# Kernel optimization log

Measured on AMD Instinct MI355X. Metric: run time of the kernel, lower is better.

## Reference

```python
import jax, jax.numpy as jnp
from jax import lax
import numpy as np

BN_EPS = 1e-5


def _dwconv3x3(x, w):
    # x: [B,C,H,W], w: [C,1,3,3] depthwise (groups == C)
    return lax.conv_general_dilated(
        x, w, window_strides=(1, 1), padding='SAME',
        dimension_numbers=('NCHW', 'OIHW', 'NCHW'),
        feature_group_count=x.shape[1])


def _bn_eval(x, g, b, m, v):
    s = g * lax.rsqrt(v + BN_EPS)            # [C]
    return x * s[None, :, None, None] + (b - m * s)[None, :, None, None]


def _maxpool2(x):
    return lax.reduce_window(x, -jnp.inf, lax.max,
                             (1, 1, 2, 2), (1, 1, 2, 2), 'VALID')


def setup_inputs() -> dict:
    key = jax.random.key(0)
    ks = jax.random.split(key, 8)
    B, Cin, H, W = 32, 128, 64, 64
    Hd = 256               # hidden_size
    K, Ck = 32, 8          # num categories, hidden_size // K
    sc = 0.05
    return {
        'v4_features': jax.random.normal(ks[0], (B, Cin, H, W), jnp.float32),
        'w1_dw': jax.random.normal(ks[1], (Cin, 1, 3, 3), jnp.float32) * sc,
        'w1_pw': jax.random.normal(ks[2], (Hd, Cin), jnp.float32) * sc,
        'bn1_g': jnp.ones((Hd,), jnp.float32),
        'bn1_b': jnp.zeros((Hd,), jnp.float32),
        'bn1_m': jnp.zeros((Hd,), jnp.float32),
        'bn1_v': jnp.ones((Hd,), jnp.float32),
        'w2_dw': jax.random.normal(ks[3], (Hd, 1, 3, 3), jnp.float32) * sc,
        'w2_pw': jax.random.normal(ks[4], (Hd, Hd), jnp.float32) * sc,
        'bn2_g': jnp.ones((Hd,), jnp.float32),
        'bn2_b': jnp.zeros((Hd,), jnp.float32),
        'bn2_m': jnp.zeros((Hd,), jnp.float32),
        'bn2_v': jnp.ones((Hd,), jnp.float32),
        'cat_w': jax.random.normal(ks[5], (K, Ck, Hd), jnp.float32) * sc,
        'emb_w': jax.random.normal(ks[6], (128, Hd), jnp.float32) * sc,
        'emb_b': jnp.zeros((128,), jnp.float32),
    }


def reference(v4_features, w1_dw, w1_pw, bn1_g, bn1_b, bn1_m, bn1_v,
              w2_dw, w2_pw, bn2_g, bn2_b, bn2_m, bn2_v,
              cat_w, emb_w, emb_b):
    # Block 1: depthwise 3x3 -> pointwise 1x1 -> BN -> ReLU -> maxpool2
    x = _dwconv3x3(v4_features, w1_dw)
    x = jnp.einsum('bchw,oc->bohw', x, w1_pw)
    x = _maxpool2(jax.nn.relu(_bn_eval(x, bn1_g, bn1_b, bn1_m, bn1_v)))
    # Block 2
    x = _dwconv3x3(x, w2_dw)
    x = jnp.einsum('bchw,oc->bohw', x, w2_pw)
    x = _maxpool2(jax.nn.relu(_bn_eval(x, bn2_g, bn2_b, bn2_m, bn2_v)))
    # All 32 category 1x1 convs fused into one batched contraction.
    # cat_spikes: [B, K, Ck, H', W'] (non-SNN branch returns raw features)
    cat_spikes = jnp.einsum('bchw,koc->bkohw', x, cat_w)
    cat_pooled = cat_spikes.mean(axis=(-2, -1))         # [B, K, Ck]
    category_activations = cat_pooled.mean(axis=-1)     # [B, K]
    pooled = x.mean(axis=(-2, -1))                      # [B, Hd]
    object_embedding = pooled @ emb_w.T + emb_b         # [B, 128]
    return cat_spikes, category_activations, object_embedding, x
```

## Files before the change

### kernel.cpp

```cpp
#include <hip/hip_runtime.h>

#define BN_EPS 1e-5f

typedef float f32x4 __attribute__((ext_vector_type(4)));
typedef short short8 __attribute__((ext_vector_type(8)));
typedef unsigned short u16;

__device__ __forceinline__ u16 f2bf(float f) {
    unsigned u = __builtin_bit_cast(unsigned, f);
    unsigned r = (u + 0x7FFFu + ((u >> 16) & 1u)) >> 16;
    return (u16)r;
}
__device__ __forceinline__ float b2f(u16 h) {
    return __builtin_bit_cast(float, (unsigned)h << 16);
}

#define SWZ(row) ((((row) & 7) ^ (((row) >> 3) & 7)) << 4)

__global__ __launch_bounds__(256) void prep_bf16(
    const float* __restrict__ w1, const float* __restrict__ w2,
    const float* __restrict__ wc, u16* __restrict__ o1,
    u16* __restrict__ o2, u16* __restrict__ oc)
{
    const int idx = blockIdx.x * 256 + threadIdx.x;
    const float* src; u16* dst; int off;
    if (idx < 8192)       { src = w1; dst = o1; off = idx; }
    else if (idx < 24576) { src = w2; dst = o2; off = idx - 8192; }
    else                  { src = wc; dst = oc; off = idx - 24576; }
    const float4 v = *(const float4*)(src + 4 * (size_t)off);
    ushort4 h;
    h.x = f2bf(v.x); h.y = f2bf(v.y); h.z = f2bf(v.z); h.w = f2bf(v.w);
    *(ushort4*)(dst + 4 * (size_t)off) = h;
}

template<int HW, int LOGW, int NPL, int IPP, int CMASK>
__global__ __launch_bounds__(256) void dw_shfl(
    const float* __restrict__ in, const float* __restrict__ wts,
    u16* __restrict__ out)
{
    const int t   = threadIdx.x;
    const int LPR = HW / 4;
    const int wq  = t & (LPR - 1);
    const int w0  = wq * 4;
    const int rin = t >> (LOGW - 2);

    for (int pl = 0; pl < NPL; ++pl) {
        const int plane = blockIdx.x * NPL + pl;
        const int c     = plane & CMASK;
        float wt[9];
#pragma unroll
        for (int i = 0; i < 9; ++i) wt[i] = wts[c * 9 + i];
        const float* ip = in  + (size_t)plane * (HW * HW);
        u16*         op = out + (size_t)plane * (HW * HW);

#pragma unroll
        for (int it = 0; it < IPP; ++it) {
            const int h = it * (1024 / HW) + rin;
            const float* rp = ip + h * HW + w0;
            const float4 zero4 = make_float4(0.f, 0.f, 0.f, 0.f);
            const float4 vc = *(const float4*)rp;
            const float4 vt = (h > 0)      ? *(const float4*)(rp - HW) : zero4;
            const float4 vb = (h < HW - 1) ? *(const float4*)(rp + HW) : zero4;

            float lc = __shfl_up(vc.w, 1),  rc = __shfl_down(vc.x, 1);
            float lt = __shfl_up(vt.w, 1),  rt = __shfl_down(vt.x, 1);
            float lb = __shfl_up(vb.w, 1),  rb = __shfl_down(vb.x, 1);
            if (wq == 0)       { lc = 0.f; lt = 0.f; lb = 0.f; }
            if (wq == LPR - 1) { rc = 0.f; rt = 0.f; rb = 0.f; }

            float o0 = 0.f, o1 = 0.f, o2 = 0.f, o3 = 0.f;
            o0 = fmaf(lt,   wt[0], fmaf(vt.x, wt[1], fmaf(vt.y, wt[2], o0)));
            o1 = fmaf(vt.x, wt[0], fmaf(vt.y, wt[1], fmaf(vt.z, wt[2], o1)));
            o2 = fmaf(vt.y, wt[0], fmaf(vt.z, wt[1], fmaf(vt.w, wt[2], o2)));
            o3 = fmaf(vt.z, wt[0], fmaf(vt.w, wt[1], fmaf(rt,   wt[2], o3)));
            o0 = fmaf(lc,   wt[3], fmaf(vc.x, wt[4], fmaf(vc.y, wt[5], o0)));
            o1 = fmaf(vc.x, wt[3], fmaf(vc.y, wt[4], fmaf(vc.z, wt[5], o1)));
            o2 = fmaf(vc.y, wt[3], fmaf(vc.z, wt[4], fmaf(vc.w, wt[5], o2)));
            o3 = fmaf(vc.z, wt[3], fmaf(vc.w, wt[4], fmaf(rc,   wt[5], o3)));
            o0 = fmaf(lb,   wt[6], fmaf(vb.x, wt[7], fmaf(vb.y, wt[8], o0)));
            o1 = fmaf(vb.x, wt[6], fmaf(vb.y, wt[7], fmaf(vb.z, wt[8], o1)));
            o2 = fmaf(vb.y, wt[6], fmaf(vb.z, wt[7], fmaf(vb.w, wt[8], o2)));
            o3 = fmaf(vb.z, wt[6], fmaf(vb.w, wt[7], fmaf(rb,   wt[8], o3)));

            ushort4 st;
            st.x = f2bf(o0); st.y = f2bf(o1); st.z = f2bf(o2); st.w = f2bf(o3);
            *(ushort4*)(op + h * HW + w0) = st;
        }
    }
}

__global__ __launch_bounds__(256, 2) void pw1_v2(
    const u16* __restrict__ t1b, const u16* __restrict__ wsW1,
    const float* __restrict__ bg, const float* __restrict__ bb,
    const float* __restrict__ bm, const float* __restrict__ bv,
    u16* __restrict__ t2b)
{
    __shared__ __align__(16) char smem[34816];
    float* sArr = (float*)(smem + 32768);
    float* tArr = (float*)(smem + 33792);

    const int bid = blockIdx.x;
    const int b   = bid >> 5;
    const int py  = bid & 31;
    const int p0  = py * 128;
    const int t   = threadIdx.x;

    {
        const float s = bg[t] * rsqrtf(bv[t] + BN_EPS);
        sArr[t] = s;
        tArr[t] = bb[t] - bm[t] * s;
    }

    {
        const u16* xb = t1b + ((size_t)b * 128) * 4096 + p0;
        const int pg = t & 15, cg = t >> 4;
        short8 vin[8];
#pragma unroll
        for (int j = 0; j < 8; ++j)
            vin[j] = *(const short8*)(xb + (size_t)(8 * cg + j) * 4096 + 8 * pg);
#pragma unroll
        for (int k = 0; k < 8; ++k) {
            short8 ov;
            ov[0] = vin[0][k]; ov[1] = vin[1][k]; ov[2] = vin[2][k]; ov[3] = vin[3][k];
            ov[4] = vin[4][k]; ov[5] = vin[5][k]; ov[6] = vin[6][k]; ov[7] = vin[7][k];
            const int row = 8 * pg + k;
            *(short8*)(smem + ((row * 256 + cg * 16) ^ SWZ(row))) = ov;
        }
    }
    __syncthreads();

    const int lane = t & 63, wid = t >> 6;
    const int lr = lane & 15, lg = lane >> 4;
    const int wo = wid * 64;

    f32x4 acc[4][8];
#pragma unroll
    for (int m = 0; m < 4; ++m)
#pragma unroll
        for (int n = 0; n < 8; ++n) acc[m][n] = (f32x4){0.f, 0.f, 0.f, 0.f};

    const u16* wbase = wsW1 + (size_t)(wo + lr) * 128 + lg * 8;
#pragma unroll
    for (int ks = 0; ks < 4; ++ks) {
        short8 af[4];
#pragma unroll
        for (int m = 0; m < 4; ++m)
            af[m] = *(const short8*)(wbase + m * 16 * 128 + ks * 32);
#pragma unroll
        for (int n = 0; n < 8; ++n) {
            const int prow = n * 16 + lr;
            const short8 bfv = *(const short8*)(smem +
                ((prow * 256 + ks * 64 + lg * 16) ^ SWZ(prow)));
#pragma unroll
            for (int m = 0; m < 4; ++m)
                acc[m][n] = __builtin_amdgcn_mfma_f32_16x16x32_bf16(af[m], bfv, acc[m][n], 0, 0, 0);
        }
    }

    u16* outb = t2b + ((size_t)(b * 256) * 32 + py) * 32;
#pragma unroll
    for (int m = 0; m < 4; ++m) {
#pragma unroll
        for (int j = 0; j < 4; ++j) {
            const int o = wo + m * 16 + 4 * lg + j;
            const float s = sArr[o], tt = tArr[o];
#pragma unroll
            for (int n = 0; n < 4; ++n) {
                const float a0 = fmaxf(fmaf(acc[m][n][j],     s, tt), 0.f);
                const float a1 = fmaxf(fmaf(acc[m][n + 4][j], s, tt), 0.f);
                const float vm = fmaxf(a0, a1);
                const float hm = fmaxf(vm, __shfl_xor(vm, 1));
                const unsigned p2 = (unsigned)f2bf(hm) |
                                    ((unsigned)f2bf(__shfl_xor(hm, 2)) << 16);
                const unsigned hi = __shfl_xor(p2, 4);
                if ((lr & 7) == 0) {
                    uint2 w2v; w2v.x = p2; w2v.y = hi;
                    *(uint2*)(outb + (size_t)o * 1024 + n * 8 + (lr >> 1)) = w2v;
                }
            }
        }
    }
}

template<int HW, int LOGW, int NPL, int IPP, int CMASK>
__global__ __launch_bounds__(256) void dw_shfl_bf(
    const u16* __restrict__ in, const float* __restrict__ wts,
    u16* __restrict__ out)
{
    const int t   = threadIdx.x;
    const int LPR = HW / 4;
    const int wq  = t & (LPR - 1);
    const int w0  = wq * 4;
    const int rin = t >> (LOGW - 2);

    for (int pl = 0; pl < NPL; ++pl) {
        const int plane = blockIdx.x * NPL + pl;
        const int c     = plane & CMASK;
        float wt[9];
#pragma unroll
        for (int i = 0; i < 9; ++i) wt[i] = wts[c * 9 + i];
        const u16* ip = in  + (size_t)plane * (HW * HW);
        u16*       op = out + (size_t)plane * (HW * HW);

#pragma unroll
        for (int it = 0; it < IPP; ++it) {
            const int h = it * (1024 / HW) + rin;
            const u16* rp = ip + h * HW + w0;
            float4 vc, vt, vb;
            {
                const ushort4 hcv = *(const ushort4*)rp;
                vc = make_float4(b2f(hcv.x), b2f(hcv.y), b2f(hcv.z), b2f(hcv.w));
            }
            if (h > 0) {
                const ushort4 htv = *(const ushort4*)(rp - HW);
                vt = make_float4(b2f(htv.x), b2f(htv.y), b2f(htv.z), b2f(htv.w));
            } else vt = make_float4(0.f, 0.f, 0.f, 0.f);
            if (h < HW - 1) {
                const ushort4 hbv = *(const ushort4*)(rp + HW);
                vb = make_float4(b2f(hbv.x), b2f(hbv.y), b2f(hbv.z), b2f(hbv.w));
            } else vb = make_float4(0.f, 0.f, 0.f, 0.f);

            float lc = __shfl_up(vc.w, 1),  rc = __shfl_down(vc.x, 1);
            float lt = __shfl_up(vt.w, 1),  rt = __shfl_down(vt.x, 1);
            float lb = __shfl_up(vb.w, 1),  rb = __shfl_down(vb.x, 1);
            if (wq == 0)       { lc = 0.f; lt = 0.f; lb = 0.f; }
            if (wq == LPR - 1) { rc = 0.f; rt = 0.f; rb = 0.f; }

            float o0 = 0.f, o1 = 0.f, o2 = 0.f, o3 = 0.f;
            o0 = fmaf(lt,   wt[0], fmaf(vt.x, wt[1], fmaf(vt.y, wt[2], o0)));
            o1 = fmaf(vt.x, wt[0], fmaf(vt.y, wt[1], fmaf(vt.z, wt[2], o1)));
            o2 = fmaf(vt.y, wt[0], fmaf(vt.z, wt[1], fmaf(vt.w, wt[2], o2)));
            o3 = fmaf(vt.z, wt[0], fmaf(vt.w, wt[1], fmaf(rt,   wt[2], o3)));
            o0 = fmaf(lc,   wt[3], fmaf(vc.x, wt[4], fmaf(vc.y, wt[5], o0)));
            o1 = fmaf(vc.x, wt[3], fmaf(vc.y, wt[4], fmaf(vc.z, wt[5], o1)));
            o2 = fmaf(vc.y, wt[3], fmaf(vc.z, wt[4], fmaf(vc.w, wt[5], o2)));
            o3 = fmaf(vc.z, wt[3], fmaf(vc.w, wt[4], fmaf(rc,   wt[5], o3)));
            o0 = fmaf(lb,   wt[6], fmaf(vb.x, wt[7], fmaf(vb.y, wt[8], o0)));
            o1 = fmaf(vb.x, wt[6], fmaf(vb.y, wt[7], fmaf(vb.z, wt[8], o1)));
            o2 = fmaf(vb.y, wt[6], fmaf(vb.z, wt[7], fmaf(vb.w, wt[8], o2)));
            o3 = fmaf(vb.z, wt[6], fmaf(vb.w, wt[7], fmaf(rb,   wt[8], o3)));

            ushort4 st;
            st.x = f2bf(o0); st.y = f2bf(o1); st.z = f2bf(o2); st.w = f2bf(o3);
            *(ushort4*)(op + h * HW + w0) = st;
        }
    }
}

__global__ __launch_bounds__(256) void pw2_mfma(
    const u16* __restrict__ t3b, const u16* __restrict__ wsW2,
    const float* __restrict__ bg, const float* __restrict__ bb,
    const float* __restrict__ bm, const float* __restrict__ bv,
    float* __restrict__ xout)
{
    __shared__ __align__(16) char smem[49664];
    float* sArr = (float*)(smem + 49152);
    float* tArr = (float*)(smem + 49408);
    float* Df   = (float*)smem;

    const int bid = blockIdx.x;
    const int o0  = ((bid >> 3) & 3) * 64;
    const int pxb = (bid >> 5) * 8 + (bid & 7);
    const int px  = pxb & 7;
    const int b   = pxb >> 3;
    const int p0  = px * 128;
    const int t   = threadIdx.x;

    const int lane = t & 63, wid = t >> 6;
    const int lr = lane & 15, lg = lane >> 4;
    const int wo = (wid >> 1) * 32;
    const int wp = (wid & 1) * 64;

    f32x4 acc[2][4];
#pragma unroll
    for (int m = 0; m < 2; ++m)
#pragma unroll
        for (int n = 0; n < 4; ++n) acc[m][n] = (f32x4){0.f, 0.f, 0.f, 0.f};

#pragma unroll
    for (int ko = 0; ko < 2; ++ko) {
        if (ko) __syncthreads();

#pragma unroll
        for (int i = 0; i < 4; ++i) {
            const int li = i * 256 + t;
            const int ol = li >> 4;
            const int f8 = li & 15;
            const short8 wv = *(const short8*)(wsW2 + (size_t)(o0 + ol) * 256 + ko * 128 + 8 * f8);
            *(short8*)(smem + ((ol * 256 + f8 * 16) ^ SWZ(ol))) = wv;
        }

        {
            const u16* xb = t3b + ((size_t)b * 256 + ko * 128) * 1024 + p0;
            const int pg = t & 15, cg = t >> 4;
            short8 vin[8];
#pragma unroll
            for (int j = 0; j < 8; ++j)
                vin[j] = *(const short8*)(xb + (size_t)(8 * cg + j) * 1024 + 8 * pg);
#pragma unroll
            for (int k = 0; k < 8; ++k) {
                short8 ov;
                ov[0] = vin[0][k]; ov[1] = vin[1][k]; ov[2] = vin[2][k]; ov[3] = vin[3][k];
                ov[4] = vin[4][k]; ov[5] = vin[5][k]; ov[6] = vin[6][k]; ov[7] = vin[7][k];
                const int row = 8 * pg + k;
                *(short8*)(smem + 16384 + ((row * 256 + cg * 16) ^ SWZ(row))) = ov;
            }
        }

        if (ko == 0 && t < 64) {
            const int o = o0 + t;
            const float s = bg[o] * rsqrtf(bv[o] + BN_EPS);
            sArr[t] = s;
            tArr[t] = bb[o] - bm[o] * s;
        }
        __syncthreads();

#pragma unroll
        for (int ks = 0; ks < 4; ++ks) {
            short8 af[2];
#pragma unroll
            for (int m = 0; m < 2; ++m) {
                const int rowm = wo + m * 16 + lr;
                af[m] = *(const short8*)(smem + ((rowm * 256 + ks * 64 + lg * 16) ^ SWZ(rowm)));
            }
#pragma unroll
            for (int n = 0; n < 4; ++n) {
                const int prow = wp + n * 16 + lr;
                const short8 bfv = *(const short8*)(smem + 16384 +
                    ((prow * 256 + ks * 64 + lg * 16) ^ SWZ(prow)));
                acc[0][n] = __builtin_amdgcn_mfma_f32_16x16x32_bf16(af[0], bfv, acc[0][n], 0, 0, 0);
                acc[1][n] = __builtin_amdgcn_mfma_f32_16x16x32_bf16(af[1], bfv, acc[1][n], 0, 0, 0);
            }
        }
    }
    __syncthreads();

    float sv[2][4], tv[2][4];
#pragma unroll
    for (int m = 0; m < 2; ++m)
#pragma unroll
        for (int j = 0; j < 4; ++j) {
            const int ol = wo + m * 16 + 4 * lg + j;
            sv[m][j] = sArr[ol];
            tv[m][j] = tArr[ol];
        }
#pragma unroll
    for (int m = 0; m < 2; ++m)
#pragma unroll
        for (int n = 0; n < 4; ++n)
#pragma unroll
            for (int j = 0; j < 4; ++j) {
                const int ol = wo + m * 16 + 4 * lg + j;
                const int pl = wp + n * 16 + lr;
                const float val = fmaf(acc[m][n][j], sv[m][j], tv[m][j]);
                Df[ol * 130 + pl] = fmaxf(val, 0.f);
            }
    __syncthreads();

#pragma unroll
    for (int i = 0; i < 8; ++i) {
        const int oi = i * 256 + t;
        const int o  = oi >> 5;
        const int q  = oi & 31;
        const int prl = q >> 4;
        const int pc  = q & 15;
        const float a0 = Df[o * 130 + prl * 64 + 2 * pc];
        const float a1 = Df[o * 130 + prl * 64 + 2 * pc + 1];
        const float b0 = Df[o * 130 + prl * 64 + 32 + 2 * pc];
        const float b1 = Df[o * 130 + prl * 64 + 32 + 2 * pc + 1];
        xout[(((size_t)(b * 256 + o0 + o)) * 16 + 2 * px + prl) * 16 + pc] =
            fmaxf(fmaxf(a0, a1), fmaxf(b0, b1));
    }
}

__global__ __launch_bounds__(256) void cat_mfma(
    const float* __restrict__ x, const u16* __restrict__ wsWc,
    float* __restrict__ spikes, float* __restrict__ cat_act)
{
    __shared__ __align__(16) char smem[36864];
    __shared__ float cs[4][32];
    __shared__ float msum[32];

    const int bid = blockIdx.x;
    const int b   = bid & 31;
    const int m0  = (bid >> 5) * 32;
    const int t   = threadIdx.x;

    const int lane = t & 63, wid = t >> 6;
    const int lr = lane & 15, lg = lane >> 4;
    const int wp = wid * 64;

    f32x4 acc[2][4];
#pragma unroll
    for (int m = 0; m < 2; ++m)
#pragma unroll
        for (int n = 0; n < 4; ++n) acc[m][n] = (f32x4){0.f, 0.f, 0.f, 0.f};

    const float* xb = x + (size_t)b * 65536;

#pragma unroll
    for (int ks = 0; ks < 4; ++ks) {
        if (ks) __syncthreads();

        {
            const int ol = t >> 3;
            const int f8 = t & 7;
            const short8 wv = *(const short8*)(wsWc + (size_t)(m0 + ol) * 256 + ks * 64 + 8 * f8);
            *(short8*)(smem + ((ol * 128 + f8 * 16) ^ SWZ(ol))) = wv;
        }

#pragma unroll
        for (int i = 0; i < 4; ++i) {
            const int li = i * 256 + t;
            const int c4 = li >> 6;
            const int f4 = li & 63;
            float4 v0 = *(const float4*)(xb + (size_t)(ks * 64 + 4 * c4 + 0) * 256 + 4 * f4);
            float4 v1 = *(const float4*)(xb + (size_t)(ks * 64 + 4 * c4 + 1) * 256 + 4 * f4);
            float4 v2 = *(const float4*)(xb + (size_t)(ks * 64 + 4 * c4 + 2) * 256 + 4 * f4);
            float4 v3 = *(const float4*)(xb + (size_t)(ks * 64 + 4 * c4 + 3) * 256 + 4 * f4);
            ushort4 h0, h1, h2, h3;
            h0.x = f2bf(v0.x); h0.y = f2bf(v1.x); h0.z = f2bf(v2.x); h0.w = f2bf(v3.x);
            h1.x = f2bf(v0.y); h1.y = f2bf(v1.y); h1.z = f2bf(v2.y); h1.w = f2bf(v3.y);
            h2.x = f2bf(v0.z); h2.y = f2bf(v1.z); h2.z = f2bf(v2.z); h2.w = f2bf(v3.z);
            h3.x = f2bf(v0.w); h3.y = f2bf(v1.w); h3.z = f2bf(v2.w); h3.w = f2bf(v3.w);
            const int p_0 = 4 * f4;
            *(ushort4*)(smem + 4096 + (((p_0 + 0) * 128 + 8 * c4) ^ SWZ(p_0 + 0))) = h0;
            *(ushort4*)(smem + 4096 + (((p_0 + 1) * 128 + 8 * c4) ^ SWZ(p_0 + 1))) = h1;
            *(ushort4*)(smem + 4096 + (((p_0 + 2) * 128 + 8 * c4) ^ SWZ(p_0 + 2))) = h2;
            *(ushort4*)(smem + 4096 + (((p_0 + 3) * 128 + 8 * c4) ^ SWZ(p_0 + 3))) = h3;
        }
        __syncthreads();

#pragma unroll
        for (int kk = 0; kk < 2; ++kk) {
            short8 af[2];
#pragma unroll
            for (int m = 0; m < 2; ++m) {
                const int rowm = m * 16 + lr;
                af[m] = *(const short8*)(smem + ((rowm * 128 + kk * 64 + lg * 16) ^ SWZ(rowm)));
            }
#pragma unroll
            for (int n = 0; n < 4; ++n) {
                const int prow = wp + n * 16 + lr;
                const short8 bfv = *(const short8*)(smem + 4096 +
                    ((prow * 128 + kk * 64 + lg * 16) ^ SWZ(prow)));
                acc[0][n] = __builtin_amdgcn_mfma_f32_16x16x32_bf16(af[0], bfv, acc[0][n], 0, 0, 0);
                acc[1][n] = __builtin_amdgcn_mfma_f32_16x16x32_bf16(af[1], bfv, acc[1][n], 0, 0, 0);
            }
        }
    }

#pragma unroll
    for (int mi = 0; mi < 2; ++mi) {
#pragma unroll
        for (int j = 0; j < 4; ++j) {
            const int m = m0 + mi * 16 + 4 * lg + j;
#pragma unroll
            for (int n = 0; n < 4; ++n)
                spikes[((size_t)(b * 256 + m)) * 256 + wp + n * 16 + lr] = acc[mi][n][j];
            float s = acc[mi][0][j] + acc[mi][1][j] + acc[mi][2][j] + acc[mi][3][j];
            s += __shfl_xor(s, 1, 64);
            s += __shfl_xor(s, 2, 64);
            s += __shfl_xor(s, 4, 64);
            s += __shfl_xor(s, 8, 64);
            if (lr == 0) cs[wid][mi * 16 + 4 * lg + j] = s;
        }
    }
    __syncthreads();
    if (t < 32) msum[t] = cs[0][t] + cs[1][t] + cs[2][t] + cs[3][t];
    __syncthreads();
    if (t < 4) {
        float s = 0.f;
#pragma unroll
        for (int o = 0; o < 8; ++o) s += msum[t * 8 + o];
        cat_act[b * 32 + (m0 >> 3) + t] = s * (1.0f / 2048.0f);
    }
}

__global__ __launch_bounds__(256) void final_kernel(
    const float* __restrict__ x,
    const float* __restrict__ embw, const float* __restrict__ embb,
    float* __restrict__ emb)
{
    const int b = blockIdx.x;
    const int t = threadIdx.x;
    __shared__ __align__(16) float pooled[256];

    {
        const float4* src = (const float4*)(x + (size_t)b * 65536 + (size_t)t * 256);
        float s = 0.f;
#pragma unroll 8
        for (int i = 0; i < 64; ++i) {
            const float4 v = src[i];
            s += v.x + v.y + v.z + v.w;
        }
        pooled[t] = s * (1.0f / 256.0f);
    }
    __syncthreads();

    if (t < 128) {
        const float4* wr = (const float4*)(embw + (size_t)t * 256);
        float d = 0.f;
#pragma unroll 8
        for (int i = 0; i < 64; ++i) {
            const float4 wv = wr[i];
            const float4 pv = *(const float4*)&pooled[4 * i];
            d = fmaf(wv.x, pv.x, d);
            d = fmaf(wv.y, pv.y, d);
            d = fmaf(wv.z, pv.z, d);
            d = fmaf(wv.w, pv.w, d);
        }
        emb[b * 128 + t] = d + embb[t];
    }
}

extern "C" void kernel_launch(void* const* d_in, const int* in_sizes, int n_in,
                              void* d_out, int out_size, void* d_ws, size_t ws_size,
                              hipStream_t stream) {
    const float* v4   = (const float*)d_in[0];
    const float* w1dw = (const float*)d_in[1];
    const float* w1pw = (const float*)d_in[2];
    const float* bn1g = (const float*)d_in[3];
    const float* bn1b = (const float*)d_in[4];
    const float* bn1m = (const float*)d_in[5];
    const float* bn1v = (const float*)d_in[6];
    const float* w2dw = (const float*)d_in[7];
    const float* w2pw = (const float*)d_in[8];
    const float* bn2g = (const float*)d_in[9];
    const float* bn2b = (const float*)d_in[10];
    const float* bn2m = (const float*)d_in[11];
    const float* bn2v = (const float*)d_in[12];
    const float* catw = (const float*)d_in[13];
    const float* embw = (const float*)d_in[14];
    const float* embb = (const float*)d_in[15];

    float* out        = (float*)d_out;
    float* cat_spikes = out;
    float* cat_act    = out + 2097152;
    float* emb        = out + 2098176;
    float* xout       = out + 2102272;

    char* ws = (char*)d_ws;
    u16* wsW1 = (u16*)ws;
    u16* wsW2 = (u16*)(ws + 65536);
    u16* wsWc = (u16*)(ws + 196608);
    u16* t1b  = (u16*)(ws + 327680);
    u16* t2b  = (u16*)(ws + 327680 + 33554432);
    u16* t3b  = (u16*)(ws + 327680 + 33554432 + 16777216);

    prep_bf16<<<160, 256, 0, stream>>>(w1pw, w2pw, catw, wsW1, wsW2, wsWc);
    dw_shfl<64, 6, 1, 4, 127><<<4096, 256, 0, stream>>>(v4, w1dw, t1b);
    pw1_v2<<<1024, 256, 0, stream>>>(t1b, wsW1, bn1g, bn1b, bn1m, bn1v, t2b);
    dw_shfl_bf<32, 5, 4, 1, 255><<<2048, 256, 0, stream>>>(t2b, w2dw, t3b);
    pw2_mfma<<<1024, 256, 0, stream>>>(t3b, wsW2, bn2g, bn2b, bn2m, bn2v, xout);
    cat_mfma<<<256, 256, 0, stream>>>(xout, wsWc, cat_spikes, cat_act);
    final_kernel<<<32, 256, 0, stream>>>(xout, embw, embb, emb);
}
```

Baseline: 110.7 us.

## Merge weight prep into dw1 launch and split cat kernel across pixel quarters

The weight bf16 conversion is folded into the first depthwise kernel as extra blocks, removing one kernel launch. The category contraction is restructured to run on 1024 blocks, each covering a quarter of the pixels with the full K=256 staged in shared memory at once. This raises parallelism and removes the per-K-step syncs. Partial category sums go to a workspace and are reduced in final_kernel. The cost is a small extra workspace round trip, larger shared memory per block, and each x tile being loaded by 8 blocks.

```diff
diff --git a/kernel.cpp b/kernel.cpp
--- a/kernel.cpp
+++ b/kernel.cpp
@@ -17,75 +17,71 @@
 
 #define SWZ(row) ((((row) & 7) ^ (((row) >> 3) & 7)) << 4)
 
-__global__ __launch_bounds__(256) void prep_bf16(
+__global__ __launch_bounds__(256) void dw1_prep(
+    const float* __restrict__ in, const float* __restrict__ wts,
+    u16* __restrict__ out,
     const float* __restrict__ w1, const float* __restrict__ w2,
     const float* __restrict__ wc, u16* __restrict__ o1,
     u16* __restrict__ o2, u16* __restrict__ oc)
 {
-    const int idx = blockIdx.x * 256 + threadIdx.x;
-    const float* src; u16* dst; int off;
-    if (idx < 8192)       { src = w1; dst = o1; off = idx; }
-    else if (idx < 24576) { src = w2; dst = o2; off = idx - 8192; }
-    else                  { src = wc; dst = oc; off = idx - 24576; }
-    const float4 v = *(const float4*)(src + 4 * (size_t)off);
-    ushort4 h;
-    h.x = f2bf(v.x); h.y = f2bf(v.y); h.z = f2bf(v.z); h.w = f2bf(v.w);
-    *(ushort4*)(dst + 4 * (size_t)off) = h;
-}
-
-template<int HW, int LOGW, int NPL, int IPP, int CMASK>
-__global__ __launch_bounds__(256) void dw_shfl(
-    const float* __restrict__ in, const float* __restrict__ wts,
-    u16* __restrict__ out)
-{
-    const int t   = threadIdx.x;
-    const int LPR = HW / 4;
-    const int wq  = t & (LPR - 1);
+    const int t = threadIdx.x;
+    if (blockIdx.x >= 4096) {
+        const int idx = (blockIdx.x - 4096) * 256 + t;
+        const float* src; u16* dst; int off;
+        if (idx < 8192)       { src = w1; dst = o1; off = idx; }
+        else if (idx < 24576) { src = w2; dst = o2; off = idx - 8192; }
+        else                  { src = wc; dst = oc; off = idx - 24576; }
+        const float4 v = *(const float4*)(src + 4 * (size_t)off);
+        ushort4 h;
+        h.x = f2bf(v.x); h.y = f2bf(v.y); h.z = f2bf(v.z); h.w = f2bf(v.w);
+        *(ushort4*)(dst + 4 * (size_t)off) = h;
+        return;
+    }
+
+    const int HW = 64;
+    const int wq  = t & 15;
     const int w0  = wq * 4;
-    const int rin = t >> (LOGW - 2);
-
-    for (int pl = 0; pl < NPL; ++pl) {
-        const int plane = blockIdx.x * NPL + pl;
-        const int c     = plane & CMASK;
-        float wt[9];
-#pragma unroll
-        for (int i = 0; i < 9; ++i) wt[i] = wts[c * 9 + i];
-        const float* ip = in  + (size_t)plane * (HW * HW);
-        u16*         op = out + (size_t)plane * (HW * HW);
-
-#pragma unroll
-        for (int it = 0; it < IPP; ++it) {
-            const int h = it * (1024 / HW) + rin;
-            const float* rp = ip + h * HW + w0;
-            const float4 zero4 = make_float4(0.f, 0.f, 0.f, 0.f);
-            const float4 vc = *(const float4*)rp;
-            const float4 vt = (h > 0)      ? *(const float4*)(rp - HW) : zero4;
-            const float4 vb = (h < HW - 1) ? *(const float4*)(rp + HW) : zero4;
-
-            float lc = __shfl_up(vc.w, 1),  rc = __shfl_down(vc.x, 1);
-            float lt = __shfl_up(vt.w, 1),  rt = __shfl_down(vt.x, 1);
-            float lb = __shfl_up(vb.w, 1),  rb = __shfl_down(vb.x, 1);
-            if (wq == 0)       { lc = 0.f; lt = 0.f; lb = 0.f; }
-            if (wq == LPR - 1) { rc = 0.f; rt = 0.f; rb = 0.f; }
-
-            float o0 = 0.f, o1 = 0.f, o2 = 0.f, o3 = 0.f;
-            o0 = fmaf(lt,   wt[0], fmaf(vt.x, wt[1], fmaf(vt.y, wt[2], o0)));
-            o1 = fmaf(vt.x, wt[0], fmaf(vt.y, wt[1], fmaf(vt.z, wt[2], o1)));
-            o2 = fmaf(vt.y, wt[0], fmaf(vt.z, wt[1], fmaf(vt.w, wt[2], o2)));
-            o3 = fmaf(vt.z, wt[0], fmaf(vt.w, wt[1], fmaf(rt,   wt[2], o3)));
-            o0 = fmaf(lc,   wt[3], fmaf(vc.x, wt[4], fmaf(vc.y, wt[5], o0)));
-            o1 = fmaf(vc.x, wt[3], fmaf(vc.y, wt[4], fmaf(vc.z, wt[5], o1)));
-            o2 = fmaf(vc.y, wt[3], fmaf(vc.z, wt[4], fmaf(vc.w, wt[5], o2)));
-            o3 = fmaf(vc.z, wt[3], fmaf(vc.w, wt[4], fmaf(rc,   wt[5], o3)));
-            o0 = fmaf(lb,   wt[6], fmaf(vb.x, wt[7], fmaf(vb.y, wt[8], o0)));
-            o1 = fmaf(vb.x, wt[6], fmaf(vb.y, wt[7], fmaf(vb.z, wt[8], o1)));
-            o2 = fmaf(vb.y, wt[6], fmaf(vb.z, wt[7], fmaf(vb.w, wt[8], o2)));
-            o3 = fmaf(vb.z, wt[6], fmaf(vb.w, wt[7], fmaf(rb,   wt[8], o3)));
-
-            ushort4 st;
-            st.x = f2bf(o0); st.y = f2bf(o1); st.z = f2bf(o2); st.w = f2bf(o3);
-            *(ushort4*)(op + h * HW + w0) = st;
-        }
+    const int rin = t >> 4;
+    const int plane = blockIdx.x;
+    const int c     = plane & 127;
+    float wt[9];
+#pragma unroll
+    for (int i = 0; i < 9; ++i) wt[i] = wts[c * 9 + i];
+    const float* ip = in  + (size_t)plane * (HW * HW);
+    u16*         op = out + (size_t)plane * (HW * HW);
+
+#pragma unroll
+    for (int it = 0; it < 4; ++it) {
+        const int h = it * 16 + rin;
+        const float* rp = ip + h * HW + w0;
+        const float4 zero4 = make_float4(0.f, 0.f, 0.f, 0.f);
+        const float4 vc = *(const float4*)rp;
+        const float4 vt = (h > 0)      ? *(const float4*)(rp - HW) : zero4;
+        const float4 vb = (h < HW - 1) ? *(const float4*)(rp + HW) : zero4;
+
+        float lc = __shfl_up(vc.w, 1),  rc = __shfl_down(vc.x, 1);
+        float lt = __shfl_up(vt.w, 1),  rt = __shfl_down(vt.x, 1);
+        float lb = __shfl_up(vb.w, 1),  rb = __shfl_down(vb.x, 1);
+        if (wq == 0)  { lc = 0.f; lt = 0.f; lb = 0.f; }
+        if (wq == 15) { rc = 0.f; rt = 0.f; rb = 0.f; }
+
+        float o0 = 0.f, o1v = 0.f, o2v = 0.f, o3v = 0.f;
+        o0  = fmaf(lt,   wt[0], fmaf(vt.x, wt[1], fmaf(vt.y, wt[2], o0)));
+        o1v = fmaf(vt.x, wt[0], fmaf(vt.y, wt[1], fmaf(vt.z, wt[2], o1v)));
+        o2v = fmaf(vt.y, wt[0], fmaf(vt.z, wt[1], fmaf(vt.w, wt[2], o2v)));
+        o3v = fmaf(vt.z, wt[0], fmaf(vt.w, wt[1], fmaf(rt,   wt[2], o3v)));
+        o0  = fmaf(lc,   wt[3], fmaf(vc.x, wt[4], fmaf(vc.y, wt[5], o0)));
+        o1v = fmaf(vc.x, wt[3], fmaf(vc.y, wt[4], fmaf(vc.z, wt[5], o1v)));
+        o2v = fmaf(vc.y, wt[3], fmaf(vc.z, wt[4], fmaf(vc.w, wt[5], o2v)));
+        o3v = fmaf(vc.z, wt[3], fmaf(vc.w, wt[4], fmaf(rc,   wt[5], o3v)));
+        o0  = fmaf(lb,   wt[6], fmaf(vb.x, wt[7], fmaf(vb.y, wt[8], o0)));
+        o1v = fmaf(vb.x, wt[6], fmaf(vb.y, wt[7], fmaf(vb.z, wt[8], o1v)));
+        o2v = fmaf(vb.y, wt[6], fmaf(vb.z, wt[7], fmaf(vb.w, wt[8], o2v)));
+        o3v = fmaf(vb.z, wt[6], fmaf(vb.w, wt[7], fmaf(rb,   wt[8], o3v)));
+
+        ushort4 st;
+        st.x = f2bf(o0); st.y = f2bf(o1v); st.z = f2bf(o2v); st.w = f2bf(o3v);
+        *(ushort4*)(op + h * HW + w0) = st;
     }
 }
 
@@ -373,80 +369,70 @@
     }
 }
 
-__global__ __launch_bounds__(256) void cat_mfma(
+__global__ __launch_bounds__(256) void cat_v2(
     const float* __restrict__ x, const u16* __restrict__ wsWc,
-    float* __restrict__ spikes, float* __restrict__ cat_act)
+    float* __restrict__ spikes, float* __restrict__ csws)
 {
-    __shared__ __align__(16) char smem[36864];
-    __shared__ float cs[4][32];
-    __shared__ float msum[32];
+    __shared__ __align__(16) char smem[49664];
+    float* cs = (float*)(smem + 49152);
 
     const int bid = blockIdx.x;
-    const int b   = bid & 31;
-    const int m0  = (bid >> 5) * 32;
+    const int g   = (bid >> 6) * 8 + (bid & 7);
+    const int m0  = ((bid >> 3) & 7) * 32;
+    const int b   = g >> 2;
+    const int q   = g & 3;
+    const int px0 = q * 64;
     const int t   = threadIdx.x;
+
+#pragma unroll
+    for (int i = 0; i < 4; ++i) {
+        const int li = i * 256 + t;
+        const int ml = li >> 5, ch = li & 31;
+        const short8 wv = *(const short8*)(wsWc + (size_t)(m0 + ml) * 256 + ch * 8);
+        *(short8*)(smem + ((ml * 512 + ch * 16) ^ SWZ(ml))) = wv;
+    }
+
+    const float* xb = x + (size_t)b * 65536;
+#pragma unroll
+    for (int i = 0; i < 4; ++i) {
+        const int li = i * 256 + t;
+        const int pq = li & 15;
+        const int cg = li >> 4;
+        const float4 v0 = *(const float4*)(xb + (size_t)(4 * cg + 0) * 256 + px0 + 4 * pq);
+        const float4 v1 = *(const float4*)(xb + (size_t)(4 * cg + 1) * 256 + px0 + 4 * pq);
+        const float4 v2 = *(const float4*)(xb + (size_t)(4 * cg + 2) * 256 + px0 + 4 * pq);
+        const float4 v3 = *(const float4*)(xb + (size_t)(4 * cg + 3) * 256 + px0 + 4 * pq);
+        ushort4 h0, h1, h2, h3;
+        h0.x = f2bf(v0.x); h0.y = f2bf(v1.x); h0.z = f2bf(v2.x); h0.w = f2bf(v3.x);
+        h1.x = f2bf(v0.y); h1.y = f2bf(v1.y); h1.z = f2bf(v2.y); h1.w = f2bf(v3.y);
+        h2.x = f2bf(v0.z); h2.y = f2bf(v1.z); h2.z = f2bf(v2.z); h2.w = f2bf(v3.z);
+        h3.x = f2bf(v0.w); h3.y = f2bf(v1.w); h3.z = f2bf(v2.w); h3.w = f2bf(v3.w);
+        const int p_ = 4 * pq;
+        *(ushort4*)(smem + 16384 + (((p_ + 0) * 512 + cg * 8) ^ SWZ(p_ + 0))) = h0;
+        *(ushort4*)(smem + 16384 + (((p_ + 1) * 512 + cg * 8) ^ SWZ(p_ + 1))) = h1;
+        *(ushort4*)(smem + 16384 + (((p_ + 2) * 512 + cg * 8) ^ SWZ(p_ + 2))) = h2;
+        *(ushort4*)(smem + 16384 + (((p_ + 3) * 512 + cg * 8) ^ SWZ(p_ + 3))) = h3;
+    }
+    __syncthreads();
 
     const int lane = t & 63, wid = t >> 6;
     const int lr = lane & 15, lg = lane >> 4;
-    const int wp = wid * 64;
-
-    f32x4 acc[2][4];
-#pragma unroll
-    for (int m = 0; m < 2; ++m)
-#pragma unroll
-        for (int n = 0; n < 4; ++n) acc[m][n] = (f32x4){0.f, 0.f, 0.f, 0.f};
-
-    const float* xb = x + (size_t)b * 65536;
-
-#pragma unroll
-    for (int ks = 0; ks < 4; ++ks) {
-        if (ks) __syncthreads();
-
-        {
-            const int ol = t >> 3;
-            const int f8 = t & 7;
-            const short8 wv = *(const short8*)(wsWc + (size_t)(m0 + ol) * 256 + ks * 64 + 8 * f8);
-            *(short8*)(smem + ((ol * 128 + f8 * 16) ^ SWZ(ol))) = wv;
-        }
-
-#pragma unroll
-        for (int i = 0; i < 4; ++i) {
-            const int li = i * 256 + t;
-            const int c4 = li >> 6;
-            const int f4 = li & 63;
-            float4 v0 = *(const float4*)(xb + (size_t)(ks * 64 + 4 * c4 + 0) * 256 + 4 * f4);
-            float4 v1 = *(const float4*)(xb + (size_t)(ks * 64 + 4 * c4 + 1) * 256 + 4 * f4);
-            float4 v2 = *(const float4*)(xb + (size_t)(ks * 64 + 4 * c4 + 2) * 256 + 4 * f4);
-            float4 v3 = *(const float4*)(xb + (size_t)(ks * 64 + 4 * c4 + 3) * 256 + 4 * f4);
-            ushort4 h0, h1, h2, h3;
-            h0.x = f2bf(v0.x); h0.y = f2bf(v1.x); h0.z = f2bf(v2.x); h0.w = f2bf(v3.x);
-            h1.x = f2bf(v0.y); h1.y = f2bf(v1.y); h1.z = f2bf(v2.y); h1.w = f2bf(v3.y);
-            h2.x = f2bf(v0.z); h2.y = f2bf(v1.z); h2.z = f2bf(v2.z); h2.w = f2bf(v3.z);
-            h3.x = f2bf(v0.w); h3.y = f2bf(v1.w); h3.z = f2bf(v2.w); h3.w = f2bf(v3.w);
-            const int p_0 = 4 * f4;
-            *(ushort4*)(smem + 4096 + (((p_0 + 0) * 128 + 8 * c4) ^ SWZ(p_0 + 0))) = h0;
-            *(ushort4*)(smem + 4096 + (((p_0 + 1) * 128 + 8 * c4) ^ SWZ(p_0 + 1))) = h1;
-            *(ushort4*)(smem + 4096 + (((p_0 + 2) * 128 + 8 * c4) ^ SWZ(p_0 + 2))) = h2;
-            *(ushort4*)(smem + 4096 + (((p_0 + 3) * 128 + 8 * c4) ^ SWZ(p_0 + 3))) = h3;
-        }
-        __syncthreads();
-
-#pragma unroll
-        for (int kk = 0; kk < 2; ++kk) {
-            short8 af[2];
-#pragma unroll
-            for (int m = 0; m < 2; ++m) {
-                const int rowm = m * 16 + lr;
-                af[m] = *(const short8*)(smem + ((rowm * 128 + kk * 64 + lg * 16) ^ SWZ(rowm)));
-            }
-#pragma unroll
-            for (int n = 0; n < 4; ++n) {
-                const int prow = wp + n * 16 + lr;
-                const short8 bfv = *(const short8*)(smem + 4096 +
-                    ((prow * 128 + kk * 64 + lg * 16) ^ SWZ(prow)));
-                acc[0][n] = __builtin_amdgcn_mfma_f32_16x16x32_bf16(af[0], bfv, acc[0][n], 0, 0, 0);
-                acc[1][n] = __builtin_amdgcn_mfma_f32_16x16x32_bf16(af[1], bfv, acc[1][n], 0, 0, 0);
-            }
+
+    f32x4 acc[2];
+    acc[0] = (f32x4){0.f, 0.f, 0.f, 0.f};
+    acc[1] = (f32x4){0.f, 0.f, 0.f, 0.f};
+
+#pragma unroll
+    for (int ks = 0; ks < 8; ++ks) {
+        const int prow = wid * 16 + lr;
+        const short8 b8 = *(const short8*)(smem + 16384 +
+            ((prow * 512 + ks * 64 + lg * 16) ^ SWZ(prow)));
+#pragma unroll
+        for (int mi = 0; mi < 2; ++mi) {
+            const int rowm = mi * 16 + lr;
+            const short8 a8 = *(const short8*)(smem +
+                ((rowm * 512 + ks * 64 + lg * 16) ^ SWZ(rowm)));
+            acc[mi] = __builtin_amdgcn_mfma_f32_16x16x32_bf16(a8, b8, acc[mi], 0, 0, 0);
         }
     }
 
@@ -454,33 +440,28 @@
     for (int mi = 0; mi < 2; ++mi) {
 #pragma unroll
         for (int j = 0; j < 4; ++j) {
-            const int m = m0 + mi * 16 + 4 * lg + j;
-#pragma unroll
-            for (int n = 0; n < 4; ++n)
-                spikes[((size_t)(b * 256 + m)) * 256 + wp + n * 16 + lr] = acc[mi][n][j];
-            float s = acc[mi][0][j] + acc[mi][1][j] + acc[mi][2][j] + acc[mi][3][j];
+            const int m  = m0 + mi * 16 + 4 * lg + j;
+            const int px = px0 + wid * 16 + lr;
+            spikes[((size_t)(b * 256 + m)) * 256 + px] = acc[mi][j];
+            float s = acc[mi][j];
             s += __shfl_xor(s, 1, 64);
             s += __shfl_xor(s, 2, 64);
             s += __shfl_xor(s, 4, 64);
             s += __shfl_xor(s, 8, 64);
-            if (lr == 0) cs[wid][mi * 16 + 4 * lg + j] = s;
+            if (lr == 0) cs[wid * 32 + mi * 16 + 4 * lg + j] = s;
         }
     }
     __syncthreads();
-    if (t < 32) msum[t] = cs[0][t] + cs[1][t] + cs[2][t] + cs[3][t];
-    __syncthreads();
-    if (t < 4) {
-        float s = 0.f;
-#pragma unroll
-        for (int o = 0; o < 8; ++o) s += msum[t * 8 + o];
-        cat_act[b * 32 + (m0 >> 3) + t] = s * (1.0f / 2048.0f);
+    if (t < 32) {
+        const float p = cs[t] + cs[32 + t] + cs[64 + t] + cs[96 + t];
+        csws[((size_t)(b * 256 + m0 + t)) * 4 + q] = p;
     }
 }
 
 __global__ __launch_bounds__(256) void final_kernel(
-    const float* __restrict__ x,
+    const float* __restrict__ x, const float* __restrict__ csws,
     const float* __restrict__ embw, const float* __restrict__ embb,
-    float* __restrict__ emb)
+    float* __restrict__ cat_act, float* __restrict__ emb)
 {
     const int b = blockIdx.x;
     const int t = threadIdx.x;
@@ -511,6 +492,15 @@
             d = fmaf(wv.w, pv.w, d);
         }
         emb[b * 128 + t] = d + embb[t];
+    } else if (t < 160) {
+        const int k = t - 128;
+        float s = 0.f;
+#pragma unroll
+        for (int o = 0; o < 8; ++o) {
+            const float4 qv = *(const float4*)&csws[((size_t)(b * 256 + k * 8 + o)) * 4];
+            s += qv.x + qv.y + qv.z + qv.w;
+        }
+        cat_act[b * 32 + k] = s * (1.0f / 2048.0f);
     }
 }
 
@@ -547,12 +537,13 @@
     u16* t1b  = (u16*)(ws + 327680);
     u16* t2b  = (u16*)(ws + 327680 + 33554432);
     u16* t3b  = (u16*)(ws + 327680 + 33554432 + 16777216);
-
-    prep_bf16<<<160, 256, 0, stream>>>(w1pw, w2pw, catw, wsW1, wsW2, wsWc);
-    dw_shfl<64, 6, 1, 4, 127><<<4096, 256, 0, stream>>>(v4, w1dw, t1b);
+    float* csws = (float*)(ws + 327680 + 33554432 + 16777216 + 16777216);
+
+    dw1_prep<<<4256, 256, 0, stream>>>(v4, w1dw, t1b, w1pw, w2pw, catw,
+                                       wsW1, wsW2, wsWc);
     pw1_v2<<<1024, 256, 0, stream>>>(t1b, wsW1, bn1g, bn1b, bn1m, bn1v, t2b);
     dw_shfl_bf<32, 5, 4, 1, 255><<<2048, 256, 0, stream>>>(t2b, w2dw, t3b);
     pw2_mfma<<<1024, 256, 0, stream>>>(t3b, wsW2, bn2g, bn2b, bn2m, bn2v, xout);
-    cat_mfma<<<256, 256, 0, stream>>>(xout, wsWc, cat_spikes, cat_act);
-    final_kernel<<<32, 256, 0, stream>>>(xout, embw, embb, emb);
-}
+    cat_v2<<<1024, 256, 0, stream>>>(xout, wsWc, cat_spikes, csws);
+    final_kernel<<<32, 256, 0, stream>>>(xout, csws, embw, embb, cat_act, emb);
+}
```

After: 102.8 us, median of 2. 7.1% less time.
